# Kernel optimization log

Measured on AMD Instinct MI355X. Metric: run time of the kernel, lower is better.

## Reference

```python
import jax, jax.numpy as jnp
import numpy as np
import math

B, I, O, D, H = 32, 1152, 10, 16, 10
SUB = 0.8
S = math.ceil(SUB * I)  # 922 subset size


def _safe_l2norm(x, axis, keepdims=False):
    # L2 norm with zero-safe gradient (forward-identical to jnp.linalg.norm)
    s = jnp.sum(x * x, axis=axis, keepdims=keepdims)
    return jnp.where(s == 0, 0.0, jnp.sqrt(jnp.where(s == 0, 1.0, s)))


def setup_inputs() -> dict:
    key = jax.random.key(0)
    k1, k2 = jax.random.split(key)
    u_predict = jax.random.normal(k1, (B, I, O, D), dtype=jnp.float32)
    # emulate torch.rand(...).topk(S, dim=1).indices: top-S distinct indices along input_caps
    noise = jax.random.uniform(k2, (B, I, O, H))
    sample_idx = jnp.argsort(-noise, axis=1)[:, :S].astype(jnp.int64)  # [B,S,O,H]
    return {"u_predict": u_predict, "sample_idx": sample_idx}


def reference(u_predict, sample_idx):
    b, i, o, d = u_predict.shape
    h = sample_idx.shape[-1]
    # scatter 0/1 hypothesis mask r: [B,I,O,H]
    bi = jnp.arange(b)[:, None, None, None]
    oi = jnp.arange(o)[None, None, :, None]
    hi = jnp.arange(h)[None, None, None, :]
    r = jnp.zeros((b, i, o, h), u_predict.dtype).at[bi, sample_idx, oi, hi].set(1.0)

    # Vr = V_exp * r; since r is 0/1, ||Vr||_D = r * ||V||_D
    Vnorm = _safe_l2norm(u_predict, axis=3)            # [B,I,O]
    Vr_norm = Vnorm[..., None] * r                     # [B,I,O,H]
    # Mu = sum_i(Vr_norm * Vr) / sum_i Vr_norm  (Vr_norm*Vr = r*||V||*V since r^2=r)
    num = jnp.einsum('bioh,biod->bodh', Vr_norm, u_predict)   # [B,O,D,H]
    Mu = num / jnp.sum(Vr_norm, axis=1)[:, :, None, :]        # [B,O,D,H]

    # losses = sum_i ||V_exp - Mu||_D  -> [B,O,H]
    diff = u_predict[..., None] - Mu[:, None]          # [B,I,O,D,H]
    losses = jnp.sum(_safe_l2norm(diff, axis=3), axis=1)
    min_idx = jnp.argmin(losses, axis=2)               # [B,O]

    # pick best hypothesis's mask per (batch, output_caps)
    final_r = jnp.take_along_axis(r, min_idx[:, None, :, None], axis=3)  # [B,I,O,1]

    # capsule weighted average
    u = u_predict * final_r
    un = _safe_l2norm(u, axis=3, keepdims=True)        # [B,I,O,1]
    v = jnp.sum(u * un, axis=1) / jnp.sum(un, axis=1)  # [B,O,D]
    return v
```

## Files before the change

kernel.cpp:

```cpp
#include <hip/hip_runtime.h>
#include <math.h>


#define B_    32
#define I_    1152
#define O_    10
#define D_    16
#define H_    10
#define S_    922
#define MASKW 36
#define NT    384
#define NW    6
#define RPT   3
#define HH    11
#define NSLOT 8
#define SCH   116
#define K0NT  256
#define MWORDS (O_ * H_ * MASKW)

template <int CTRL, int ROWM>
static __device__ __forceinline__ float dpp_f(float v) {
    return __int_as_float(__builtin_amdgcn_update_dpp(
        0, __float_as_int(v), CTRL, ROWM, 0xf, true));
}
static __device__ __forceinline__ float wave_sum_f32(float v) {
    v += dpp_f<0x111, 0xf>(v);
    v += dpp_f<0x112, 0xf>(v);
    v += dpp_f<0x114, 0xf>(v);
    v += dpp_f<0x118, 0xf>(v);
    v += dpp_f<0x142, 0xa>(v);
    v += dpp_f<0x143, 0xc>(v);
    return v;
}
template <int CTRL, int ROWM>
static __device__ __forceinline__ double dpp_d(double v) {
    long long x = __double_as_longlong(v);
    int lo = (int)(unsigned)(x & 0xffffffffLL);
    int hi = (int)(x >> 32);
    lo = __builtin_amdgcn_update_dpp(0, lo, CTRL, ROWM, 0xf, true);
    hi = __builtin_amdgcn_update_dpp(0, hi, CTRL, ROWM, 0xf, true);
    return __longlong_as_double((long long)(unsigned)lo | ((long long)hi << 32));
}
static __device__ __forceinline__ double wave_sum_f64(double v) {
    v += dpp_d<0x111, 0xf>(v);
    v += dpp_d<0x112, 0xf>(v);
    v += dpp_d<0x114, 0xf>(v);
    v += dpp_d<0x118, 0xf>(v);
    v += dpp_d<0x142, 0xa>(v);
    v += dpp_d<0x143, 0xc>(v);
    return v;
}

__global__ __launch_bounds__(K0NT, 2) void ransac_masks(
    const int*  __restrict__ sidx,
    unsigned*   __restrict__ maskG)
{
    __shared__ unsigned lm[MWORDS];
    const int blk = blockIdx.x;
    const int b = blk & 31, k = blk >> 5;
    const int tid = threadIdx.x;

    for (int t = tid; t < MWORDS; t += K0NT) lm[t] = 0u;
    __syncthreads();

    const int s0  = k * SCH;
    const int cnt = min(S_ - s0, SCH);
    const int n4  = cnt * 25;
    const int4* base = (const int4*)(sidx + (size_t)b * (S_ * O_ * H_)
                                          + (size_t)s0 * (O_ * H_));
    for (int j4 = tid; j4 < n4; j4 += K0NT) {
        int4 v = base[j4];
        int vv[4] = {v.x, v.y, v.z, v.w};
        int j = j4 * 4;
        #pragma unroll
        for (int e = 0; e < 4; ++e) {
            int jj  = j + e;
            int rem = jj % 100;
            int o   = rem / 10;
            int h   = rem - 10 * o;
            int val = vv[e];
            atomicOr(&lm[(o * H_ + h) * MASKW + (val >> 5)], 1u << (val & 31));
        }
    }
    __syncthreads();

    unsigned* dst = maskG + (size_t)blk * MWORDS;
    for (int t = tid; t < MWORDS; t += K0NT) dst[t] = lm[t];
}

__global__ __launch_bounds__(NT, 3) void ransac_main(
    const float*    __restrict__ up,
    const unsigned* __restrict__ maskG,
    float*          __restrict__ out)
{
    __shared__ unsigned                 mask[H_][MASKW];
    __shared__ __align__(16) float      hred[HH][NW][20];
    __shared__ float                    Mu_s[H_][D_];
    __shared__ double                   lpart[H_][NW];
    __shared__ double                   losses[H_];
    __shared__ int                      hstar;

    const int blk = blockIdx.x;
    const int xcd = blk & 7, g = blk >> 3;
    const int gg  = g / O_;
    const int b   = xcd + 8 * gg;
    const int o   = g - O_ * gg;
    const int bo  = b * O_ + o;

    const int tid  = threadIdx.x;
    const int lane = tid & 63;
    const int wv   = tid >> 6;

    unsigned mw8[NSLOT];
    const bool mt = tid < H_ * MASKW;
    if (mt) {
        #pragma unroll
        for (int k = 0; k < NSLOT; ++k)
            mw8[k] = maskG[(size_t)(k * 32 + b) * MWORDS + o * (H_ * MASKW) + tid];
    }

    const float* ub = up + ((size_t)b * I_ * O_ + o) * D_;
    float4 R[RPT][4];
    #pragma unroll
    for (int r = 0; r < RPT; ++r) {
        const float4* p = (const float4*)(ub + (size_t)(tid + r * NT) * (O_ * D_));
        R[r][0] = p[0]; R[r][1] = p[1]; R[r][2] = p[2]; R[r][3] = p[3];
    }

    if (mt) {
        unsigned m = mw8[0];
        #pragma unroll
        for (int k = 1; k < NSLOT; ++k) m |= mw8[k];
        ((unsigned*)mask)[tid] = m;
    }

    float vn[RPT], usq[RPT];
    #pragma unroll
    for (int r = 0; r < RPT; ++r) {
        float4 q0 = R[r][0], q1 = R[r][1], q2 = R[r][2], q3 = R[r][3];
        float s = q0.x*q0.x + q0.y*q0.y + q0.z*q0.z + q0.w*q0.w
                + q1.x*q1.x + q1.y*q1.y + q1.z*q1.z + q1.w*q1.w
                + q2.x*q2.x + q2.y*q2.y + q2.z*q2.z + q2.w*q2.w
                + q3.x*q3.x + q3.y*q3.y + q3.z*q3.z + q3.w*q3.w;
        vn[r] = sqrtf(s);
        float uq[D_] = {q0.x,q0.y,q0.z,q0.w, q1.x,q1.y,q1.z,q1.w,
                        q2.x,q2.y,q2.z,q2.w, q3.x,q3.y,q3.z,q3.w};
        float t = 0.f;
        #pragma unroll
        for (int d = 0; d < D_; ++d) t = fmaf(uq[d], uq[d], t);
        usq[r] = t;
    }
    __syncthreads();

    const int      w0   = tid >> 5;
    const unsigned bitm = 1u << (tid & 31);
    for (int h = 0; h < HH; ++h) {
        float na[17];
        #pragma unroll
        for (int d = 0; d < 17; ++d) na[d] = 0.f;
        #pragma unroll
        for (int r = 0; r < RPT; ++r) {
            float w = vn[r];
            if (h < H_) {
                unsigned mw = mask[h][w0 + 12 * r];
                w = (mw & bitm) ? 0.f : w;
            }
            float4 q0 = R[r][0], q1 = R[r][1], q2 = R[r][2], q3 = R[r][3];
            na[ 0] = fmaf(w, q0.x, na[ 0]); na[ 1] = fmaf(w, q0.y, na[ 1]);
            na[ 2] = fmaf(w, q0.z, na[ 2]); na[ 3] = fmaf(w, q0.w, na[ 3]);
            na[ 4] = fmaf(w, q1.x, na[ 4]); na[ 5] = fmaf(w, q1.y, na[ 5]);
            na[ 6] = fmaf(w, q1.z, na[ 6]); na[ 7] = fmaf(w, q1.w, na[ 7]);
            na[ 8] = fmaf(w, q2.x, na[ 8]); na[ 9] = fmaf(w, q2.y, na[ 9]);
            na[10] = fmaf(w, q2.z, na[10]); na[11] = fmaf(w, q2.w, na[11]);
            na[12] = fmaf(w, q3.x, na[12]); na[13] = fmaf(w, q3.y, na[13]);
            na[14] = fmaf(w, q3.z, na[14]); na[15] = fmaf(w, q3.w, na[15]);
            na[16] += w;
        }
        #pragma unroll
        for (int d = 0; d < 17; ++d) na[d] = wave_sum_f32(na[d]);
        if (lane == 63) {
            *(float4*)&hred[h][wv][ 0] = make_float4(na[ 0], na[ 1], na[ 2], na[ 3]);
            *(float4*)&hred[h][wv][ 4] = make_float4(na[ 4], na[ 5], na[ 6], na[ 7]);
            *(float4*)&hred[h][wv][ 8] = make_float4(na[ 8], na[ 9], na[10], na[11]);
            *(float4*)&hred[h][wv][12] = make_float4(na[12], na[13], na[14], na[15]);
            hred[h][wv][16] = na[16];
        }
    }
    __syncthreads();

    for (int h = wv; h < H_; h += NW) {
        if (lane < D_) {
            float naj = 0.f, totj = 0.f, na16 = 0.f, tot16 = 0.f;
            #pragma unroll
            for (int w = 0; w < NW; ++w) {
                naj   += hred[h ][w][lane];
                totj  += hred[10][w][lane];
                na16  += hred[h ][w][16];
                tot16 += hred[10][w][16];
            }
            float rd = 1.f / (tot16 - na16);
            Mu_s[h][lane] = (totj - naj) * rd;
        }
    }
    __syncthreads();

    for (int h = 0; h < H_; ++h) {
        float4 m0 = *(const float4*)&Mu_s[h][0];
        float4 m1 = *(const float4*)&Mu_s[h][4];
        float4 m2 = *(const float4*)&Mu_s[h][8];
        float4 m3 = *(const float4*)&Mu_s[h][12];
        float mv[D_] = {m0.x, m0.y, m0.z, m0.w, m1.x, m1.y, m1.z, m1.w,
                        m2.x, m2.y, m2.z, m2.w, m3.x, m3.y, m3.z, m3.w};
        float musq = 0.f;
        #pragma unroll
        for (int d = 0; d < D_; ++d) musq = fmaf(mv[d], mv[d], musq);
        double l = 0.0;
        #pragma unroll
        for (int r = 0; r < RPT; ++r) {
            float uq[D_] = {R[r][0].x, R[r][0].y, R[r][0].z, R[r][0].w,
                            R[r][1].x, R[r][1].y, R[r][1].z, R[r][1].w,
                            R[r][2].x, R[r][2].y, R[r][2].z, R[r][2].w,
                            R[r][3].x, R[r][3].y, R[r][3].z, R[r][3].w};
            float dot = 0.f;
            #pragma unroll
            for (int d = 0; d < D_; ++d) dot = fmaf(uq[d], mv[d], dot);
            float d2 = fmaf(-2.f, dot, usq[r] + musq);
            l += (double)sqrtf(fmaxf(d2, 0.f));
        }
        l = wave_sum_f64(l);
        if (lane == 63) lpart[h][wv] = l;
    }
    __syncthreads();

    if (tid < H_) {
        double t = 0.0;
        #pragma unroll
        for (int w = 0; w < NW; ++w) t += lpart[tid][w];
        losses[tid] = t;
    }
    __syncthreads();
    if (tid == 0) {
        int best = 0; double bl = losses[0];
        #pragma unroll
        for (int h = 1; h < H_; ++h)
            if (losses[h] < bl) { bl = losses[h]; best = h; }
        hstar = best;
    }
    __syncthreads();
    if (tid < D_)
        out[(size_t)bo * D_ + tid] = Mu_s[hstar][tid];
}

extern "C" void kernel_launch(void* const* d_in, const int* in_sizes, int n_in,
                              void* d_out, int out_size, void* d_ws, size_t ws_size,
                              hipStream_t stream) {
    const float* up   = (const float*)d_in[0];
    const int*   sidx = (const int*)d_in[1];
    float*       out  = (float*)d_out;
    unsigned*    maskG = (unsigned*)d_ws;
    ransac_masks<<<NSLOT * B_, K0NT, 0, stream>>>(sidx, maskG);
    ransac_main<<<B_ * O_, NT, 0, stream>>>(up, maskG, out);
}
```

Baseline: 110.5 us.

## Split main kernel into scan, loss, and pick kernels over half-row blocks

Replaces the single 384-thread-per-(b,o) kernel with three kernels. Two kernels (scan and loss) each launch 640 single-wave blocks, with each block covering half of the input capsules. Partial hypothesis sums and losses go through global workspace, and a final small kernel picks the argmin hypothesis. The intent is to remove intra-block barriers and shared-memory reductions and to spread the work across more independent blocks. The cost is two extra launches, re-reading u_predict in the loss kernel, and higher register pressure from 9 rows per thread.

```diff
diff --git a/kernel.cpp b/kernel.cpp
--- a/kernel.cpp
+++ b/kernel.cpp
@@ -9,14 +9,17 @@
 #define H_    10
 #define S_    922
 #define MASKW 36
-#define NT    384
-#define NW    6
-#define RPT   3
 #define HH    11
-#define NSLOT 8
+#define NPAIR 320
+#define HROWS 576
+#define RPT   9
+#define K0NT  256
 #define SCH   116
-#define K0NT  256
 #define MWORDS (O_ * H_ * MASKW)
+#define HSTRIDE 20
+
+#define WS_HRED_OFF 0x500000u
+#define WS_LOSS_OFF 0x600000u
 
 template <int CTRL, int ROWM>
 static __device__ __forceinline__ float dpp_f(float v) {
@@ -49,6 +52,13 @@
     v += dpp_d<0x142, 0xa>(v);
     v += dpp_d<0x143, 0xc>(v);
     return v;
+}
+
+static __device__ __forceinline__ void task_bo(int p, int& b, int& o) {
+    int xcd = p & 7, g = p >> 3;
+    int gg = g / O_;
+    b = xcd + 8 * gg;
+    o = g - O_ * gg;
 }
 
 __global__ __launch_bounds__(K0NT, 2) void ransac_masks(
@@ -88,53 +98,40 @@
     for (int t = tid; t < MWORDS; t += K0NT) dst[t] = lm[t];
 }
 
-__global__ __launch_bounds__(NT, 3) void ransac_main(
+__global__ __launch_bounds__(64, 1) void ransac_scan(
     const float*    __restrict__ up,
     const unsigned* __restrict__ maskG,
-    float*          __restrict__ out)
+    float*          __restrict__ hredG)
 {
-    __shared__ unsigned                 mask[H_][MASKW];
-    __shared__ __align__(16) float      hred[HH][NW][20];
-    __shared__ float                    Mu_s[H_][D_];
-    __shared__ double                   lpart[H_][NW];
-    __shared__ double                   losses[H_];
-    __shared__ int                      hstar;
-
-    const int blk = blockIdx.x;
-    const int xcd = blk & 7, g = blk >> 3;
-    const int gg  = g / O_;
-    const int b   = xcd + 8 * gg;
-    const int o   = g - O_ * gg;
-    const int bo  = b * O_ + o;
-
-    const int tid  = threadIdx.x;
-    const int lane = tid & 63;
-    const int wv   = tid >> 6;
-
-    unsigned mw8[NSLOT];
-    const bool mt = tid < H_ * MASKW;
-    if (mt) {
-        #pragma unroll
-        for (int k = 0; k < NSLOT; ++k)
-            mw8[k] = maskG[(size_t)(k * 32 + b) * MWORDS + o * (H_ * MASKW) + tid];
+    __shared__ unsigned mask[H_][HROWS / 32];
+
+    const int blk  = blockIdx.x;
+    const int half = (blk >= NPAIR) ? 1 : 0;
+    const int p    = blk - NPAIR * half;
+    int b, o; task_bo(p, b, o);
+    const int r0  = half * HROWS;
+    const int tid = threadIdx.x;
+
+    for (int w = tid; w < H_ * (HROWS / 32); w += 64) {
+        int h  = w / 18;
+        int lw = w - 18 * h;
+        unsigned m = 0u;
+        #pragma unroll
+        for (int k = 0; k < 8; ++k)
+            m |= maskG[(size_t)(k * 32 + b) * MWORDS
+                       + (o * H_ + h) * MASKW + half * 18 + lw];
+        mask[h][lw] = m;
     }
 
     const float* ub = up + ((size_t)b * I_ * O_ + o) * D_;
     float4 R[RPT][4];
     #pragma unroll
     for (int r = 0; r < RPT; ++r) {
-        const float4* p = (const float4*)(ub + (size_t)(tid + r * NT) * (O_ * D_));
-        R[r][0] = p[0]; R[r][1] = p[1]; R[r][2] = p[2]; R[r][3] = p[3];
-    }
-
-    if (mt) {
-        unsigned m = mw8[0];
-        #pragma unroll
-        for (int k = 1; k < NSLOT; ++k) m |= mw8[k];
-        ((unsigned*)mask)[tid] = m;
-    }
-
-    float vn[RPT], usq[RPT];
+        const float4* pr = (const float4*)(ub + (size_t)(r0 + tid + 64 * r) * (O_ * D_));
+        R[r][0] = pr[0]; R[r][1] = pr[1]; R[r][2] = pr[2]; R[r][3] = pr[3];
+    }
+
+    float vn[RPT];
     #pragma unroll
     for (int r = 0; r < RPT; ++r) {
         float4 q0 = R[r][0], q1 = R[r][1], q2 = R[r][2], q3 = R[r][3];
@@ -143,12 +140,6 @@
                 + q2.x*q2.x + q2.y*q2.y + q2.z*q2.z + q2.w*q2.w
                 + q3.x*q3.x + q3.y*q3.y + q3.z*q3.z + q3.w*q3.w;
         vn[r] = sqrtf(s);
-        float uq[D_] = {q0.x,q0.y,q0.z,q0.w, q1.x,q1.y,q1.z,q1.w,
-                        q2.x,q2.y,q2.z,q2.w, q3.x,q3.y,q3.z,q3.w};
-        float t = 0.f;
-        #pragma unroll
-        for (int d = 0; d < D_; ++d) t = fmaf(uq[d], uq[d], t);
-        usq[r] = t;
     }
     __syncthreads();
 
@@ -162,7 +153,7 @@
         for (int r = 0; r < RPT; ++r) {
             float w = vn[r];
             if (h < H_) {
-                unsigned mw = mask[h][w0 + 12 * r];
+                unsigned mw = mask[h][w0 + 2 * r];
                 w = (mw & bitm) ? 0.f : w;
             }
             float4 q0 = R[r][0], q1 = R[r][1], q2 = R[r][2], q3 = R[r][3];
@@ -178,31 +169,64 @@
         }
         #pragma unroll
         for (int d = 0; d < 17; ++d) na[d] = wave_sum_f32(na[d]);
-        if (lane == 63) {
-            *(float4*)&hred[h][wv][ 0] = make_float4(na[ 0], na[ 1], na[ 2], na[ 3]);
-            *(float4*)&hred[h][wv][ 4] = make_float4(na[ 4], na[ 5], na[ 6], na[ 7]);
-            *(float4*)&hred[h][wv][ 8] = make_float4(na[ 8], na[ 9], na[10], na[11]);
-            *(float4*)&hred[h][wv][12] = make_float4(na[12], na[13], na[14], na[15]);
-            hred[h][wv][16] = na[16];
+        if (tid == 63) {
+            float* dst = hredG + (size_t)blk * (HH * HSTRIDE) + h * HSTRIDE;
+            *(float4*)(dst +  0) = make_float4(na[ 0], na[ 1], na[ 2], na[ 3]);
+            *(float4*)(dst +  4) = make_float4(na[ 4], na[ 5], na[ 6], na[ 7]);
+            *(float4*)(dst +  8) = make_float4(na[ 8], na[ 9], na[10], na[11]);
+            *(float4*)(dst + 12) = make_float4(na[12], na[13], na[14], na[15]);
+            dst[16] = na[16];
         }
     }
-    __syncthreads();
-
-    for (int h = wv; h < H_; h += NW) {
-        if (lane < D_) {
-            float naj = 0.f, totj = 0.f, na16 = 0.f, tot16 = 0.f;
-            #pragma unroll
-            for (int w = 0; w < NW; ++w) {
-                naj   += hred[h ][w][lane];
-                totj  += hred[10][w][lane];
-                na16  += hred[h ][w][16];
-                tot16 += hred[10][w][16];
-            }
-            float rd = 1.f / (tot16 - na16);
-            Mu_s[h][lane] = (totj - naj) * rd;
-        }
-    }
-    __syncthreads();
+}
+
+__global__ __launch_bounds__(64, 1) void ransac_loss(
+    const float* __restrict__ up,
+    const float* __restrict__ hredG,
+    double*      __restrict__ lossG)
+{
+    __shared__ float               comb[HH][17];
+    __shared__ __align__(16) float Mu_s[H_][D_];
+
+    const int blk  = blockIdx.x;
+    const int half = (blk >= NPAIR) ? 1 : 0;
+    const int p    = blk - NPAIR * half;
+    int b, o; task_bo(p, b, o);
+    const int r0  = half * HROWS;
+    const int tid = threadIdx.x;
+
+    const float* ub = up + ((size_t)b * I_ * O_ + o) * D_;
+    float4 R[RPT][4];
+    #pragma unroll
+    for (int r = 0; r < RPT; ++r) {
+        const float4* pr = (const float4*)(ub + (size_t)(r0 + tid + 64 * r) * (O_ * D_));
+        R[r][0] = pr[0]; R[r][1] = pr[1]; R[r][2] = pr[2]; R[r][3] = pr[3];
+    }
+
+    for (int t = tid; t < HH * 17; t += 64) {
+        int h = t / 17, d = t - 17 * h;
+        comb[h][d] = hredG[(size_t)p            * (HH * HSTRIDE) + h * HSTRIDE + d]
+                   + hredG[(size_t)(NPAIR + p) * (HH * HSTRIDE) + h * HSTRIDE + d];
+    }
+    __syncthreads();
+    for (int t = tid; t < H_ * D_; t += 64) {
+        int h = t >> 4, d = t & 15;
+        float rd = 1.f / (comb[10][16] - comb[h][16]);
+        Mu_s[h][d] = (comb[10][d] - comb[h][d]) * rd;
+    }
+    __syncthreads();
+
+    float usq[RPT];
+    #pragma unroll
+    for (int r = 0; r < RPT; ++r) {
+        float4 q0 = R[r][0], q1 = R[r][1], q2 = R[r][2], q3 = R[r][3];
+        float uq[D_] = {q0.x,q0.y,q0.z,q0.w, q1.x,q1.y,q1.z,q1.w,
+                        q2.x,q2.y,q2.z,q2.w, q3.x,q3.y,q3.z,q3.w};
+        float t = 0.f;
+        #pragma unroll
+        for (int d = 0; d < D_; ++d) t = fmaf(uq[d], uq[d], t);
+        usq[r] = t;
+    }
 
     for (int h = 0; h < H_; ++h) {
         float4 m0 = *(const float4*)&Mu_s[h][0];
@@ -228,27 +252,44 @@
             l += (double)sqrtf(fmaxf(d2, 0.f));
         }
         l = wave_sum_f64(l);
-        if (lane == 63) lpart[h][wv] = l;
-    }
-    __syncthreads();
-
-    if (tid < H_) {
-        double t = 0.0;
-        #pragma unroll
-        for (int w = 0; w < NW; ++w) t += lpart[tid][w];
-        losses[tid] = t;
-    }
+        if (tid == 63) lossG[(size_t)blk * H_ + h] = l;
+    }
+}
+
+__global__ __launch_bounds__(64, 8) void ransac_pick(
+    const double* __restrict__ lossG,
+    const float*  __restrict__ hredG,
+    float*        __restrict__ out)
+{
+    __shared__ double lc[H_];
+    __shared__ int    hstar;
+    const int p = blockIdx.x;
+    int b, o; task_bo(p, b, o);
+    const int tid = threadIdx.x;
+
+    if (tid < H_)
+        lc[tid] = lossG[(size_t)p * H_ + tid]
+                + lossG[(size_t)(NPAIR + p) * H_ + tid];
     __syncthreads();
     if (tid == 0) {
-        int best = 0; double bl = losses[0];
+        int best = 0; double bl = lc[0];
         #pragma unroll
         for (int h = 1; h < H_; ++h)
-            if (losses[h] < bl) { bl = losses[h]; best = h; }
+            if (lc[h] < bl) { bl = lc[h]; best = h; }
         hstar = best;
     }
     __syncthreads();
-    if (tid < D_)
-        out[(size_t)bo * D_ + tid] = Mu_s[hstar][tid];
+    if (tid < D_) {
+        const float* s0 = hredG + (size_t)p            * (HH * HSTRIDE);
+        const float* s1 = hredG + (size_t)(NPAIR + p) * (HH * HSTRIDE);
+        int hs = hstar;
+        float c10d = s0[10 * HSTRIDE + tid] + s1[10 * HSTRIDE + tid];
+        float chd  = s0[hs * HSTRIDE + tid] + s1[hs * HSTRIDE + tid];
+        float c10s = s0[10 * HSTRIDE + 16]  + s1[10 * HSTRIDE + 16];
+        float chs  = s0[hs * HSTRIDE + 16]  + s1[hs * HSTRIDE + 16];
+        float rd = 1.f / (c10s - chs);
+        out[((size_t)b * O_ + o) * D_ + tid] = (c10d - chd) * rd;
+    }
 }
 
 extern "C" void kernel_launch(void* const* d_in, const int* in_sizes, int n_in,
@@ -257,7 +298,11 @@
     const float* up   = (const float*)d_in[0];
     const int*   sidx = (const int*)d_in[1];
     float*       out  = (float*)d_out;
-    unsigned*    maskG = (unsigned*)d_ws;
-    ransac_masks<<<NSLOT * B_, K0NT, 0, stream>>>(sidx, maskG);
-    ransac_main<<<B_ * O_, NT, 0, stream>>>(up, maskG, out);
-}
+    unsigned* maskG = (unsigned*)d_ws;
+    float*    hredG = (float*)((char*)d_ws + WS_HRED_OFF);
+    double*   lossG = (double*)((char*)d_ws + WS_LOSS_OFF);
+    ransac_masks<<<8 * B_,     K0NT, 0, stream>>>(sidx, maskG);
+    ransac_scan <<<2 * NPAIR,  64,   0, stream>>>(up, maskG, hredG);
+    ransac_loss <<<2 * NPAIR,  64,   0, stream>>>(up, hredG, lossG);
+    ransac_pick <<<NPAIR,      64,   0, stream>>>(lossG, hredG, out);
+}
```

Result: faster. 106.7 us (-3.4%).
